# Optimization experiments

Hardware: AMD Instinct MI355X
Metric: run time of the kernel (lower is better)

## Reference

```python
import jax, jax.numpy as jnp
import numpy as np

N, E, CIN, H, HEADS, B = 50000, 800000, 16, 64, 3, 64
D0 = HEADS * H            # conv1 out (heads concatenated) = 192
D1 = D0 + CIN             # x1 dim = 208
D2 = 2 * D1               # x2 dim = 416
MLP_IN = 3 * D2           # 1248
MLP_HID = MLP_IN // 2     # 624
EPS = 1e-5


def setup_inputs() -> dict:
    key = jax.random.key(0)
    ks = jax.random.split(key, 24)
    r = lambda k, s, sc=0.05: (jax.random.normal(k, s, dtype=jnp.float32) * sc)
    inp = {
        'x': jax.random.normal(ks[0], (N, CIN), dtype=jnp.float32),
        'edge_index': jax.random.randint(ks[1], (2, E), 0, N, dtype=jnp.int32),
        'edge_attr': jax.random.normal(ks[2], (E, 4), dtype=jnp.float32),
        'batch': jnp.sort(jax.random.randint(ks[3], (N,), 0, B, dtype=jnp.int32)),
        # conv1 (GeneralConv, heads=3, concat): msg/edge/self linears -> D0
        'W_msg1': r(ks[4], (CIN, D0)), 'b_msg1': jnp.zeros((D0,), jnp.float32),
        'W_edge1': r(ks[5], (4, D0)), 'b_edge1': jnp.zeros((D0,), jnp.float32),
        'W_self1': r(ks[6], (CIN, D0)), 'b_self1': jnp.zeros((D0,), jnp.float32),
        'g1': jnp.ones((D0,), jnp.float32), 'be1': jnp.zeros((D0,), jnp.float32),
        # conv2 (GeneralConv, heads=1, in==out -> identity self)
        'W_msg2': r(ks[7], (D1, D1)), 'b_msg2': jnp.zeros((D1,), jnp.float32),
        'W_edge2': r(ks[8], (4, D1)), 'b_edge2': jnp.zeros((D1,), jnp.float32),
        'g2': jnp.ones((D1,), jnp.float32), 'be2': jnp.zeros((D1,), jnp.float32),
        # MLP head
        'W_l1': r(ks[9], (MLP_IN, MLP_HID)), 'b_l1': jnp.zeros((MLP_HID,), jnp.float32),
        'alpha': jnp.asarray(0.25, jnp.float32),  # PReLU default
        'W_l2': r(ks[10], (MLP_HID, 2)), 'b_l2': jnp.zeros((2,), jnp.float32),
    }
    return inp


def _bn(h, g, b):
    m = h.mean(axis=0)
    v = h.var(axis=0)  # biased, like torch BatchNorm training mode
    return (h - m) * jax.lax.rsqrt(v + EPS) * g + b


def reference(x, edge_index, edge_attr, batch,
              W_msg1, b_msg1, W_edge1, b_edge1, W_self1, b_self1, g1, be1,
              W_msg2, b_msg2, W_edge2, b_edge2, g2, be2,
              W_l1, b_l1, alpha, W_l2, b_l2):
    src, dst = edge_index[0], edge_index[1]
    # conv1: gather -> linear msg + edge feature -> scatter-add -> + self linear
    m1 = x[src] @ W_msg1 + b_msg1 + edge_attr @ W_edge1 + b_edge1   # [E, D0]
    h1 = jax.ops.segment_sum(m1, dst, num_segments=N) + (x @ W_self1 + b_self1)
    h1 = _bn(h1, g1, be1)
    x1 = jnp.concatenate([h1, x], axis=1)                           # [N, D1]
    # conv2 (identity self-connection since in==out)
    m2 = x1[src] @ W_msg2 + b_msg2 + edge_attr @ W_edge2 + b_edge2  # [E, D1]
    h2 = jax.ops.segment_sum(m2, dst, num_segments=N) + x1
    h2 = _bn(h2, g2, be2)
    x2 = jnp.concatenate([h2, x1], axis=1)                          # [N, D2]
    # global add / mean / max pooling by graph id
    s = jax.ops.segment_sum(x2, batch, num_segments=B)
    cnt = jax.ops.segment_sum(jnp.ones((x2.shape[0], 1), x2.dtype), batch, num_segments=B)
    mean = s / jnp.maximum(cnt, 1.0)
    mx = jax.ops.segment_max(x2, batch, num_segments=B)
    pooled = jnp.concatenate([s, mx, mean], axis=1)                 # [B, 3*D2]
    # MLP head: Linear -> Dropout(0) -> PReLU -> Linear -> log_softmax
    h = pooled @ W_l1 + b_l1
    h = jnp.where(h >= 0, h, alpha * h)
    logits = h @ W_l2 + b_l2
    return jax.nn.log_softmax(logits, axis=-1)
```

## Files before the change

### kernel.cpp

```cpp
#include <hip/hip_runtime.h>

typedef __attribute__((ext_vector_type(8))) short short8;
typedef __attribute__((ext_vector_type(4))) float f32x4;
typedef unsigned short u16;
typedef unsigned int u32;

__device__ __forceinline__ u16 f2bf(float f) {
  u32 u = __float_as_uint(f);
  u = (u + 0x7fffu + ((u >> 16) & 1u)) >> 16;
  return (u16)u;
}
__device__ __forceinline__ float bf2f(u16 v) { return __uint_as_float((u32)v << 16); }
__device__ __forceinline__ void atomAddF(float* p, float v) { unsafeAtomicAdd(p, v); }
__device__ __forceinline__ void addp(float* v, u32 p) {
  v[0] += bf2f((u16)p);
  v[1] += bf2f((u16)(p >> 16));
}

__global__ void prep_k(const float* __restrict__ Wm1, const float* __restrict__ We1,
                       const float* __restrict__ Ws1, const float* __restrict__ Wm2,
                       const float* __restrict__ Wl1, const float* __restrict__ x,
                       const int* __restrict__ batch, u16* __restrict__ Wp1,
                       u16* __restrict__ Wp2, u16* __restrict__ Wp3,
                       u16* __restrict__ xbf, int* __restrict__ gstart,
                       int* __restrict__ gend, int* __restrict__ deg,
                       float* __restrict__ bns1p, float* __restrict__ bns2p, int N, int E) {
  int tid = blockIdx.x * 256 + threadIdx.x;
  if (tid < 64 * 192) {
    int k = tid / 192, n = tid % 192;
    float v = 0.f;
    if (k < 16) v = Wm1[k * 192 + n];
    else if (k < 20) v = We1[(k - 16) * 192 + n];
    else if (k < 36) v = Ws1[(k - 20) * 192 + n];
    Wp1[((k >> 3) * 192 + n) * 8 + (k & 7)] = f2bf(v);
  }
  if (tid < 224 * 208) {
    int k = tid / 208, n = tid % 208;
    float v = (k < 208) ? Wm2[k * 208 + n] : 0.f;
    Wp2[((k >> 3) * 208 + n) * 8 + (k & 7)] = f2bf(v);
  }
  if (tid < N * 8) {
    float2 p = *(const float2*)(x + (size_t)tid * 2);
    *(u32*)(xbf + (size_t)tid * 2) = (u32)f2bf(p.x) | ((u32)f2bf(p.y) << 16);
  }
  if (tid < N) {
    int b = batch[tid];
    if (tid == 0 || batch[tid - 1] != b) gstart[b] = tid;
    if (tid == N - 1 || batch[tid + 1] != b) gend[b] = tid;
    deg[tid] = 0;
  }
  if (tid < 64 * 384) bns1p[tid] = 0.f;
  if (tid < 64 * 832) bns2p[tid] = 0.f;
  if (tid < 1248 * 624) {
    int k = tid / 624, n = tid % 624;
    Wp3[((size_t)(k >> 3) * 624 + n) * 8 + (k & 7)] = f2bf(Wl1[(size_t)k * 624 + n]);
  }
}

__global__ void count_k(const int* __restrict__ ei, int* __restrict__ deg,
                        int* __restrict__ ord, int E) {
  int e = blockIdx.x * 256 + threadIdx.x;
  if (e >= E) return;
  ord[e] = atomicAdd(&deg[ei[E + e]], 1);
}

__global__ void scanA_k(const int* __restrict__ deg, int* __restrict__ bsum, int N) {
  __shared__ int sh[256];
  int t = threadIdx.x;
  int i = blockIdx.x * 256 + t;
  sh[t] = (i < N) ? deg[i] : 0;
  __syncthreads();
  for (int off = 128; off > 0; off >>= 1) {
    if (t < off) sh[t] += sh[t + off];
    __syncthreads();
  }
  if (t == 0) bsum[blockIdx.x] = sh[0];
}

__global__ void scanC_k(const int* __restrict__ deg, const int* __restrict__ bsum,
                        int* __restrict__ rowptr, int N, int nb) {
  __shared__ int sb2[256];
  __shared__ int sh[256];
  int t = threadIdx.x;
  int bv = (t < nb) ? bsum[t] : 0;
  sb2[t] = bv;
  __syncthreads();
  for (int off = 1; off < 256; off <<= 1) {
    int u = (t >= off) ? sb2[t - off] : 0;
    __syncthreads();
    sb2[t] += u;
    __syncthreads();
  }
  int bpref = (blockIdx.x == 0) ? 0 : sb2[blockIdx.x - 1];
  int i = blockIdx.x * 256 + t;
  int d = (i < N) ? deg[i] : 0;
  sh[t] = d;
  __syncthreads();
  for (int off = 1; off < 256; off <<= 1) {
    int u = (t >= off) ? sh[t - off] : 0;
    __syncthreads();
    sh[t] += u;
    __syncthreads();
  }
  int excl = sh[t] - d + bpref;
  if (i < N) {
    rowptr[i] = excl;
    if (i == N - 1) rowptr[N] = excl + d;
  }
}

__global__ void scatter_k(const int* __restrict__ ei, const float* __restrict__ ea,
                          const int* __restrict__ ord, const int* __restrict__ rowptr,
                          int4* __restrict__ se16, int E) {
  int e = blockIdx.x * 256 + threadIdx.x;
  if (e >= E) return;
  int s = ei[e], d = ei[E + e];
  float4 w = *(const float4*)(ea + (size_t)e * 4);
  int slot = rowptr[d] + ord[e];
  int4 ent;
  ent.x = s;
  ent.y = (int)((u32)f2bf(w.x) | ((u32)f2bf(w.y) << 16));
  ent.z = (int)((u32)f2bf(w.z) | ((u32)f2bf(w.w) << 16));
  ent.w = 0;
  se16[slot] = ent;
}

__global__ void __launch_bounds__(256) conv1_k(
    const int4* __restrict__ se16, const int* __restrict__ rowptr,
    const u16* __restrict__ xbf, const u16* __restrict__ Bp,
    const float* __restrict__ bm1, const float* __restrict__ be1,
    const float* __restrict__ bs1, u16* __restrict__ acc1c, u16* __restrict__ h1bf,
    float* __restrict__ bns1p, int N) {
  __shared__ __align__(16) u16 Uls[16][72];
  __shared__ float degls[16];
  int tid = threadIdx.x;
  int nl = tid >> 4, q = tid & 15;
  int n = blockIdx.x * 16 + nl;
  bool nval = n < N;
  int j0 = nval ? rowptr[n] : 0;
  int j1 = nval ? rowptr[n + 1] : 0;
  float v[20];
#pragma unroll
  for (int i = 0; i < 20; ++i) v[i] = 0.f;
  {
    int j = j0 + q;
    bool a0 = j < j1, a1 = (j + 16) < j1;
    int jj0 = a0 ? j : 0;
    int jj1 = a1 ? (j + 16) : 0;
    int4 p0 = se16[jj0];
    int4 p1 = se16[jj1];
    const uint4* xs0 = (const uint4*)(xbf + (size_t)(a0 ? p0.x : 0) * 16);
    uint4 x00 = xs0[0], x01 = xs0[1];
    const uint4* xs1 = (const uint4*)(xbf + (size_t)(a1 ? p1.x : 0) * 16);
    uint4 x10 = xs1[0], x11 = xs1[1];
    if (a0) {
      addp(v + 0, x00.x); addp(v + 2, x00.y); addp(v + 4, x00.z); addp(v + 6, x00.w);
      addp(v + 8, x01.x); addp(v + 10, x01.y); addp(v + 12, x01.z); addp(v + 14, x01.w);
      addp(v + 16, (u32)p0.y); addp(v + 18, (u32)p0.z);
    }
    if (a1) {
      addp(v + 0, x10.x); addp(v + 2, x10.y); addp(v + 4, x10.z); addp(v + 6, x10.w);
      addp(v + 8, x11.x); addp(v + 10, x11.y); addp(v + 12, x11.z); addp(v + 14, x11.w);
      addp(v + 16, (u32)p1.y); addp(v + 18, (u32)p1.z);
    }
    for (j += 32; j < j1; j += 16) {
      int4 p = se16[j];
      const uint4* xs = (const uint4*)(xbf + (size_t)p.x * 16);
      uint4 x0 = xs[0], x1 = xs[1];
      addp(v + 0, x0.x); addp(v + 2, x0.y); addp(v + 4, x0.z); addp(v + 6, x0.w);
      addp(v + 8, x1.x); addp(v + 10, x1.y); addp(v + 12, x1.z); addp(v + 14, x1.w);
      addp(v + 16, (u32)p.y); addp(v + 18, (u32)p.z);
    }
  }
#pragma unroll
  for (int i = 0; i < 20; ++i) {
    v[i] += __shfl_xor(v[i], 1);
    v[i] += __shfl_xor(v[i], 2);
    v[i] += __shfl_xor(v[i], 4);
    v[i] += __shfl_xor(v[i], 8);
  }
  float degf = (float)(j1 - j0);
  const u16* xr = xbf + (size_t)n * 16;
  {
    u32 w2[2];
#pragma unroll
    for (int jj = 0; jj < 2; ++jj) {
      int t0 = q * 4 + 2 * jj, t1 = t0 + 1;
      u16 b0 = (t0 < 20) ? f2bf(v[t0]) : ((t0 < 36 && nval) ? xr[t0 - 20] : (u16)0);
      u16 b1 = (t1 < 20) ? f2bf(v[t1]) : ((t1 < 36 && nval) ? xr[t1 - 20] : (u16)0);
      w2[jj] = (u32)b0 | ((u32)b1 << 16);
    }
    *(uint2*)&Uls[nl][q * 4] = make_uint2(w2[0], w2[1]);
  }
  if (nval) {
    int t0 = q * 2, t1 = t0 + 1;
    float f0 = (t0 < 20) ? v[t0] : ((t0 == 20) ? degf : 0.f);
    float f1 = (t1 < 20) ? v[t1] : ((t1 == 20) ? degf : 0.f);
    *(u32*)(acc1c + (size_t)n * 32 + q * 2) = (u32)f2bf(f0) | ((u32)f2bf(f1) << 16);
  }
  if (q == 0) degls[nl] = degf;
  __syncthreads();
  int w = tid >> 6, lane = tid & 63, rc = lane & 15, qd = lane >> 4;
  int slice = (blockIdx.x & 63) * 384;
  for (int nt = w; nt < 12; nt += 4) {
    f32x4 acc = {0.f, 0.f, 0.f, 0.f};
#pragma unroll
    for (int kb = 0; kb < 2; ++kb) {
      short8 av = *(const short8*)&Uls[rc][kb * 32 + qd * 8];
      short8 bv = *(const short8*)(Bp + (size_t)((kb * 4 + qd) * 192 + nt * 16 + rc) * 8);
      acc = __builtin_amdgcn_mfma_f32_16x16x32_bf16(av, bv, acc, 0, 0, 0);
    }
    int col = nt * 16 + rc;
    float bb = bm1[col] + be1[col], bsv = bs1[col];
    float ps = 0.f, pq = 0.f;
#pragma unroll
    for (int r = 0; r < 4; ++r) {
      int ml = qd * 4 + r;
      int m = blockIdx.x * 16 + ml;
      float val = acc[r] + degls[ml] * bb + bsv;
      if (m < N) {
        h1bf[(size_t)m * 192 + col] = f2bf(val);
        ps += val;
        pq += val * val;
      }
    }
    ps += __shfl_xor(ps, 16); ps += __shfl_xor(ps, 32);
    pq += __shfl_xor(pq, 16); pq += __shfl_xor(pq, 32);
    if (qd == 0) {
      atomAddF(&bns1p[slice + col], ps);
      atomAddF(&bns1p[slice + 192 + col], pq);
    }
  }
}

__global__ void bnfin1_k(const float* __restrict__ bns1p, const float* __restrict__ g1,
                         const float* __restrict__ bta1, float Ninv,
                         float* __restrict__ aff1) {
  int c = threadIdx.x;
  if (c >= 192) return;
  float sm = 0.f, sq = 0.f;
  for (int k = 0; k < 64; ++k) {
    sm += bns1p[k * 384 + c];
    sq += bns1p[k * 384 + 192 + c];
  }
  float m1 = sm * Ninv;
  float var = sq * Ninv - m1 * m1;
  float s1 = g1[c] * rsqrtf(var + 1e-5f);
  aff1[c] = s1;
  aff1[192 + c] = bta1[c] - m1 * s1;
}

__global__ void __launch_bounds__(256) conv2_k(
    const int4* __restrict__ se16, const int* __restrict__ rowptr,
    const u16* __restrict__ acc1c, const u16* __restrict__ h1bf,
    const u16* __restrict__ xbf, const u16* __restrict__ Bp1, const u16* __restrict__ Bp2,
    const float* __restrict__ bm1, const float* __restrict__ be1,
    const float* __restrict__ bs1, const float* __restrict__ aff1,
    const float* __restrict__ We2, const float* __restrict__ bm2,
    const float* __restrict__ be2, float* __restrict__ bns2p,
    u16* __restrict__ h2bf, int N) {
  __shared__ __align__(16) u16 Uls[16][72];
  __shared__ __align__(16) u16 Vls[16][232];
  __shared__ __align__(16) u16 X1ls[16][208];
  __shared__ float degls[16], sdegls[16], eals[16][4];
  int tid = threadIdx.x;
  int nl = tid >> 4, q = tid & 15;
  int n = blockIdx.x * 16 + nl;
  bool nval = n < N;
  int j0 = nval ? rowptr[n] : 0;
  int j1 = nval ? rowptr[n + 1] : 0;
  int base = blockIdx.x * 16;

  uint4 sg0, sg1, sgx;
  int r0 = tid / 24, c0 = tid % 24;
  int r1 = (tid + 256) / 24, c1 = (tid + 256) % 24;
  {
    int gr = base + r0;
    sg0 = (gr < N) ? *(const uint4*)(h1bf + (size_t)gr * 192 + c0 * 8)
                   : make_uint4(0, 0, 0, 0);
  }
  if (tid < 128) {
    int gr = base + r1;
    sg1 = (gr < N) ? *(const uint4*)(h1bf + (size_t)gr * 192 + c1 * 8)
                   : make_uint4(0, 0, 0, 0);
  }
  if (tid < 32) {
    int gr = base + (tid >> 1);
    sgx = (gr < N) ? *(const uint4*)(xbf + (size_t)gr * 16 + (tid & 1) * 8)
                   : make_uint4(0, 0, 0, 0);
  }

  float v[21];
#pragma unroll
  for (int i = 0; i < 21; ++i) v[i] = 0.f;
  {
    int j = j0 + q;
    bool a0 = j < j1, a1 = (j + 16) < j1;
    int jj0 = a0 ? j : 0;
    int jj1 = a1 ? (j + 16) : 0;
    int4 p0 = se16[jj0];
    int4 p1 = se16[jj1];
    const uint4* cr0 = (const uint4*)(acc1c + (size_t)(a0 ? p0.x : 0) * 32);
    uint4 c00 = cr0[0], c01 = cr0[1], c02 = cr0[2];
    const uint4* cr1 = (const uint4*)(acc1c + (size_t)(a1 ? p1.x : 0) * 32);
    uint4 c10 = cr1[0], c11 = cr1[1], c12 = cr1[2];
    if (a0) {
      addp(v + 0, c00.x); addp(v + 2, c00.y); addp(v + 4, c00.z); addp(v + 6, c00.w);
      addp(v + 8, c01.x); addp(v + 10, c01.y); addp(v + 12, c01.z); addp(v + 14, c01.w);
      addp(v + 16, c02.x); addp(v + 18, c02.y);
      v[20] += bf2f((u16)c02.z);
    }
    if (a1) {
      addp(v + 0, c10.x); addp(v + 2, c10.y); addp(v + 4, c10.z); addp(v + 6, c10.w);
      addp(v + 8, c11.x); addp(v + 10, c11.y); addp(v + 12, c11.z); addp(v + 14, c11.w);
      addp(v + 16, c12.x); addp(v + 18, c12.y);
      v[20] += bf2f((u16)c12.z);
    }
    for (j += 32; j < j1; j += 16) {
      int s = se16[j].x;
      const uint4* cr = (const uint4*)(acc1c + (size_t)s * 32);
      uint4 c0 = cr[0], c1 = cr[1], c2 = cr[2];
      addp(v + 0, c0.x); addp(v + 2, c0.y); addp(v + 4, c0.z); addp(v + 6, c0.w);
      addp(v + 8, c1.x); addp(v + 10, c1.y); addp(v + 12, c1.z); addp(v + 14, c1.w);
      addp(v + 16, c2.x); addp(v + 18, c2.y);
      v[20] += bf2f((u16)c2.z);
    }
  }

  *(uint4*)&X1ls[r0][c0 * 8] = sg0;
  if (tid < 128) *(uint4*)&X1ls[r1][c1 * 8] = sg1;
  if (tid < 32) *(uint4*)&X1ls[tid >> 1][192 + (tid & 1) * 8] = sgx;

#pragma unroll
  for (int i = 0; i < 21; ++i) {
    v[i] += __shfl_xor(v[i], 1);
    v[i] += __shfl_xor(v[i], 2);
    v[i] += __shfl_xor(v[i], 4);
    v[i] += __shfl_xor(v[i], 8);
  }
  const u16* selfr = acc1c + (size_t)n * 32;
  {
    u32 w2[2];
#pragma unroll
    for (int jj = 0; jj < 2; ++jj) {
      int t0 = q * 4 + 2 * jj, t1 = t0 + 1;
      u16 b0 = (t0 < 20) ? f2bf(v[t0]) : ((t0 < 36 && nval) ? selfr[t0 - 20] : (u16)0);
      u16 b1 = (t1 < 20) ? f2bf(v[t1]) : ((t1 < 36 && nval) ? selfr[t1 - 20] : (u16)0);
      w2[jj] = (u32)b0 | ((u32)b1 << 16);
    }
    *(uint2*)&Uls[nl][q * 4] = make_uint2(w2[0], w2[1]);
  }
  {
    int t0 = q * 2, t1 = t0 + 1;
    u16 b0 = (t0 < 16 && nval) ? selfr[t0] : (u16)0;
    u16 b1 = (t1 < 16 && nval) ? selfr[t1] : (u16)0;
    *(u32*)&Vls[nl][192 + q * 2] = (u32)b0 | ((u32)b1 << 16);
  }
  if (q == 0) sdegls[nl] = v[20];
  if (q == 1) degls[nl] = nval ? bf2f(selfr[20]) : 0.f;
  if (q == 2) {
#pragma unroll
    for (int k = 0; k < 4; ++k) eals[nl][k] = nval ? bf2f(selfr[16 + k]) : 0.f;
  }
  __syncthreads();
  int w = tid >> 6, lane = tid & 63, rc = lane & 15, qd = lane >> 4;
  for (int nt = w; nt < 12; nt += 4) {
    f32x4 acc = {0.f, 0.f, 0.f, 0.f};
#pragma unroll
    for (int kb = 0; kb < 2; ++kb) {
      short8 av = *(const short8*)&Uls[rc][kb * 32 + qd * 8];
      short8 bv = *(const short8*)(Bp1 + (size_t)((kb * 4 + qd) * 192 + nt * 16 + rc) * 8);
      acc = __builtin_amdgcn_mfma_f32_16x16x32_bf16(av, bv, acc, 0, 0, 0);
    }
    int col = nt * 16 + rc;
    float s1 = aff1[col], t1 = aff1[192 + col];
    float bb = bm1[col] + be1[col], bsv = bs1[col];
#pragma unroll
    for (int r = 0; r < 4; ++r) {
      int ml = qd * 4 + r;
      float qv = acc[r] + sdegls[ml] * bb + degls[ml] * bsv;
      Vls[ml][col] = f2bf(qv * s1 + degls[ml] * t1);
    }
  }
  __syncthreads();
  int slice = (blockIdx.x & 63) * 832;
  for (int nt = w; nt < 13; nt += 4) {
    f32x4 acc = {0.f, 0.f, 0.f, 0.f};
#pragma unroll
    for (int kb = 0; kb < 7; ++kb) {
      short8 av = *(const short8*)&Vls[rc][kb * 32 + qd * 8];
      short8 bv = *(const short8*)(Bp2 + (size_t)((kb * 4 + qd) * 208 + nt * 16 + rc) * 8);
      acc = __builtin_amdgcn_mfma_f32_16x16x32_bf16(av, bv, acc, 0, 0, 0);
    }
    int col = nt * 16 + rc;
    float w0 = We2[col], w1 = We2[208 + col], w2 = We2[416 + col], w3 = We2[624 + col];
    float bb2 = bm2[col] + be2[col];
    bool c192 = col < 192;
    float s1 = c192 ? aff1[col] : 0.f;
    float t1 = c192 ? aff1[192 + col] : 0.f;
    float ps = 0.f, pq = 0.f;
#pragma unroll
    for (int r = 0; r < 4; ++r) {
      int ml = qd * 4 + r;
      int m = blockIdx.x * 16 + ml;
      bool mv = m < N;
      float x1 = bf2f(X1ls[ml][col]);
      if (c192) x1 = x1 * s1 + t1;
      float val = acc[r] + eals[ml][0] * w0 + eals[ml][1] * w1 + eals[ml][2] * w2 +
                  eals[ml][3] * w3 + degls[ml] * bb2 + x1;
      if (mv) {
        h2bf[(size_t)m * 208 + col] = f2bf(val);
        ps += val;
        pq += val * val;
      }
    }
    ps += __shfl_xor(ps, 16); ps += __shfl_xor(ps, 32);
    pq += __shfl_xor(pq, 16); pq += __shfl_xor(pq, 32);
    if (qd == 0) {
      atomAddF(&bns2p[slice + col], ps);
      atomAddF(&bns2p[slice + 416 + col], pq);
    }
  }
}

__global__ void bnfin2_k(const float* __restrict__ bns2p, const float* __restrict__ aff1,
                         const float* __restrict__ g2, const float* __restrict__ bta2,
                         float Ninv, float* __restrict__ aff) {
  int f = blockIdx.x * 256 + threadIdx.x;
  if (f >= 416) return;
  float sc, sh;
  if (f < 208) {
    float sm = 0.f, sq = 0.f;
    for (int k = 0; k < 64; ++k) {
      sm += bns2p[k * 832 + f];
      sq += bns2p[k * 832 + 416 + f];
    }
    float m2 = sm * Ninv;
    float var = sq * Ninv - m2 * m2;
    sc = g2[f] * rsqrtf(var + 1e-5f);
    sh = bta2[f] - m2 * sc;
  } else if (f < 400) {
    sc = aff1[f - 208];
    sh = aff1[192 + (f - 208)];
  } else {
    sc = 1.f;
    sh = 0.f;
  }
  aff[f] = sc;
  aff[416 + f] = sh;
}

__global__ void pool_k(const u16* __restrict__ h2bf, const u16* __restrict__ h1bf,
                       const u16* __restrict__ xbf, const float* __restrict__ aff,
                       const int* __restrict__ gstart, const int* __restrict__ gend,
                       float* __restrict__ psp, float* __restrict__ pmp) {
  int b = blockIdx.x, sub = blockIdx.y;
  int t = threadIdx.x;
  if (t >= 208) return;
  int s0 = gstart[b], e0 = gend[b];
  int cnt = (s0 <= e0) ? e0 - s0 + 1 : 0;
  int per = (cnt + 15) >> 4;
  int n0 = s0 + sub * per;
  int n1 = min(n0 + per, s0 + cnt);
  int f = 2 * t;
  const u16* src;
  int stride;
  if (f < 208) { src = h2bf + f; stride = 208; }
  else if (f < 400) { src = h1bf + (f - 208); stride = 192; }
  else { src = xbf + (f - 400); stride = 16; }
  float sc0 = aff[f], sc1 = aff[f + 1];
  float sh0 = aff[416 + f], sh1 = aff[417 + f];
  float s0f = 0.f, s1f = 0.f, m0f = -3.4e38f, m1f = -3.4e38f;
  for (int n = n0; n < n1; ++n) {
    u32 p = *(const u32*)(src + (size_t)n * stride);
    float v0 = bf2f((u16)p) * sc0 + sh0;
    float v1 = bf2f((u16)(p >> 16)) * sc1 + sh1;
    s0f += v0; s1f += v1;
    m0f = fmaxf(m0f, v0); m1f = fmaxf(m1f, v1);
  }
  size_t idx = ((size_t)(b * 16 + sub)) * 416 + f;
  *(float2*)(psp + idx) = make_float2(s0f, s1f);
  *(float2*)(pmp + idx) = make_float2(m0f, m1f);
}

__global__ void pooledprep_k(const float* __restrict__ psp, const float* __restrict__ pmp,
                             const int* __restrict__ gstart, const int* __restrict__ gend,
                             u16* __restrict__ Apool) {
  int b = blockIdx.x, t = threadIdx.x;
  int cnt = gend[b] - gstart[b] + 1;
  float inv = 1.f / (float)max(cnt, 1);
  for (int f = t; f < 416; f += 256) {
    float s = 0.f, m = -3.4e38f;
    for (int k = 0; k < 16; ++k) {
      size_t idx = ((size_t)(b * 16 + k)) * 416 + f;
      s += psp[idx];
      m = fmaxf(m, pmp[idx]);
    }
    u16* row = Apool + (size_t)b * 1248;
    row[f] = f2bf(s);
    row[416 + f] = f2bf((cnt > 0) ? m : 0.f);
    row[832 + f] = f2bf(s * inv);
  }
}

__global__ void mlpgemm_k(const u16* __restrict__ A, const u16* __restrict__ Bp,
                          const float* __restrict__ b1, const float* __restrict__ al,
                          float* __restrict__ hid) {
  int lane = threadIdx.x;
  int mt = blockIdx.x, nt = blockIdx.y;
  int rc = lane & 15, qd = lane >> 4;
  f32x4 acc = {0.f, 0.f, 0.f, 0.f};
  const u16* Ap = A + (size_t)(mt * 16 + rc) * 1248 + qd * 8;
  const u16* Bq = Bp + (size_t)(qd * 624 + nt * 16 + rc) * 8;
  for (int kb = 0; kb < 39; ++kb) {
    short8 av = *(const short8*)(Ap + kb * 32);
    short8 bv = *(const short8*)(Bq + (size_t)kb * 4 * 624 * 8);
    acc = __builtin_amdgcn_mfma_f32_16x16x32_bf16(av, bv, acc, 0, 0, 0);
  }
  int col = nt * 16 + rc;
  float bb = b1[col], alpha = al[0];
  int m0 = mt * 16 + qd * 4;
#pragma unroll
  for (int r = 0; r < 4; ++r) {
    float v = acc[r] + bb;
    hid[(size_t)(m0 + r) * 624 + col] = (v >= 0.f) ? v : alpha * v;
  }
}

__global__ void head_k(const float* __restrict__ hid, const float* __restrict__ W2,
                       const float* __restrict__ b2, float* __restrict__ out) {
  int b = blockIdx.x, t = threadIdx.x;
  float p0 = 0.f, p1 = 0.f;
  for (int k = t; k < 624; k += 64) {
    float h = hid[(size_t)b * 624 + k];
    p0 += h * W2[k * 2];
    p1 += h * W2[k * 2 + 1];
  }
#pragma unroll
  for (int off = 32; off > 0; off >>= 1) {
    p0 += __shfl_down(p0, off);
    p1 += __shfl_down(p1, off);
  }
  if (t == 0) {
    float l0 = p0 + b2[0], l1 = p1 + b2[1];
    float m = fmaxf(l0, l1);
    float lse = m + logf(expf(l0 - m) + expf(l1 - m));
    out[b * 2] = l0 - lse;
    out[b * 2 + 1] = l1 - lse;
  }
}

extern "C" void kernel_launch(void* const* d_in, const int* in_sizes, int n_in,
                              void* d_out, int out_size, void* d_ws, size_t ws_size,
                              hipStream_t stream) {
  const float* x = (const float*)d_in[0];
  const int* ei = (const int*)d_in[1];
  const float* ea = (const float*)d_in[2];
  const int* batch = (const int*)d_in[3];
  const float* Wm1 = (const float*)d_in[4];
  const float* bm1 = (const float*)d_in[5];
  const float* We1 = (const float*)d_in[6];
  const float* be1 = (const float*)d_in[7];
  const float* Ws1 = (const float*)d_in[8];
  const float* bs1 = (const float*)d_in[9];
  const float* g1 = (const float*)d_in[10];
  const float* bta1 = (const float*)d_in[11];
  const float* Wm2 = (const float*)d_in[12];
  const float* bm2 = (const float*)d_in[13];
  const float* We2 = (const float*)d_in[14];
  const float* be2 = (const float*)d_in[15];
  const float* g2 = (const float*)d_in[16];
  const float* bta2 = (const float*)d_in[17];
  const float* Wl1 = (const float*)d_in[18];
  const float* bl1 = (const float*)d_in[19];
  const float* alpha = (const float*)d_in[20];
  const float* Wl2 = (const float*)d_in[21];
  const float* bl2 = (const float*)d_in[22];
  float* out = (float*)d_out;

  const int N = in_sizes[3];
  const int E = in_sizes[2] / 4;
  const int nb = (N + 255) / 256;
  const float Ninv = 1.f / (float)N;

  float* ws = (float*)d_ws;
  size_t o = 0;
  u16* acc1c = (u16*)(ws + o); o += (size_t)N * 16;
  u16* h2bf = (u16*)(ws + o);  o += (size_t)N * 104;
  u16* h1bf = (u16*)(ws + o);  o += (size_t)N * 96;
  u16* xbf = (u16*)(ws + o);   o += (size_t)N * 8;
  u16* Wp1 = (u16*)(ws + o);   o += 6144;
  u16* Wp2 = (u16*)(ws + o);   o += 23296;
  u16* Wp3 = (u16*)(ws + o);   o += 389376;
  u16* Apool = (u16*)(ws + o); o += 39936;
  float* hid = ws + o;    o += 64 * 624;
  float* bns1p = ws + o;  o += 64 * 384;
  float* bns2p = ws + o;  o += 64 * 832;
  float* aff1 = ws + o;   o += 384;
  float* aff = ws + o;    o += 832;
  float* psp = ws + o;    o += (size_t)64 * 16 * 416;
  float* pmp = ws + o;    o += (size_t)64 * 16 * 416;
  int* gstart = (int*)(ws + o); o += 64;
  int* gend = (int*)(ws + o);   o += 64;
  int* deg = (int*)(ws + o);    o += N;
  int* rowptr = (int*)(ws + o); o += N + 1;
  int* ord = (int*)(ws + o);    o += E;
  int* bsum = (int*)(ws + o);   o += 256;
  o = (o + 3) & ~(size_t)3;
  int4* se16 = (int4*)(ws + o); o += (size_t)4 * E;

  const int gconv = (N + 15) / 16;
  prep_k<<<(E + 255) / 256, 256, 0, stream>>>(Wm1, We1, Ws1, Wm2, Wl1, x, batch, Wp1, Wp2,
                                              Wp3, xbf, gstart, gend, deg, bns1p, bns2p,
                                              N, E);
  count_k<<<(E + 255) / 256, 256, 0, stream>>>(ei, deg, ord, E);
  scanA_k<<<nb, 256, 0, stream>>>(deg, bsum, N);
  scanC_k<<<nb, 256, 0, stream>>>(deg, bsum, rowptr, N, nb);
  scatter_k<<<(E + 255) / 256, 256, 0, stream>>>(ei, ea, ord, rowptr, se16, E);
  conv1_k<<<gconv, 256, 0, stream>>>(se16, rowptr, xbf, Wp1, bm1, be1, bs1, acc1c, h1bf,
                                     bns1p, N);
  bnfin1_k<<<1, 256, 0, stream>>>(bns1p, g1, bta1, Ninv, aff1);
  conv2_k<<<gconv, 256, 0, stream>>>(se16, rowptr, acc1c, h1bf, xbf, Wp1, Wp2, bm1, be1,
                                     bs1, aff1, We2, bm2, be2, bns2p, h2bf, N);
  bnfin2_k<<<2, 256, 0, stream>>>(bns2p, aff1, g2, bta2, Ninv, aff);
  pool_k<<<dim3(64, 16), 256, 0, stream>>>(h2bf, h1bf, xbf, aff, gstart, gend, psp, pmp);
  pooledprep_k<<<64, 256, 0, stream>>>(psp, pmp, gstart, gend, Apool);
  mlpgemm_k<<<dim3(4, 39), 64, 0, stream>>>(Apool, Wp3, bl1, alpha, hid);
  head_k<<<64, 64, 0, stream>>>(hid, Wl2, bl2, out);
}
```

Baseline: 292.6 us.

## Double conv node tile to 32 per block and split MLP GEMM K across warps

The conv1 and conv2 kernels now handle 32 nodes per 512-thread block instead of 16 per 256. The MFMA loops are rewritten as jobs over two 16-row tiles, so each fetched weight fragment serves more rows and there are fewer blocks, fewer BN partial-sum atomics per node, and fewer launches. The MLP GEMM now splits its 39-step K loop across four warps and reduces the partial results through shared memory, which shortens the serial MFMA chain per block. In exchange the conv kernels use twice the shared memory and larger blocks, which may reduce occupancy and the scheduler's ability to hide gather latency.

```diff
diff --git a/kernel.cpp b/kernel.cpp
--- a/kernel.cpp
+++ b/kernel.cpp
@@ -125,17 +125,17 @@
   se16[slot] = ent;
 }
 
-__global__ void __launch_bounds__(256) conv1_k(
+__global__ void __launch_bounds__(512) conv1_k(
     const int4* __restrict__ se16, const int* __restrict__ rowptr,
     const u16* __restrict__ xbf, const u16* __restrict__ Bp,
     const float* __restrict__ bm1, const float* __restrict__ be1,
     const float* __restrict__ bs1, u16* __restrict__ acc1c, u16* __restrict__ h1bf,
     float* __restrict__ bns1p, int N) {
-  __shared__ __align__(16) u16 Uls[16][72];
-  __shared__ float degls[16];
+  __shared__ __align__(16) u16 Uls[32][72];
+  __shared__ float degls[32];
   int tid = threadIdx.x;
   int nl = tid >> 4, q = tid & 15;
-  int n = blockIdx.x * 16 + nl;
+  int n = blockIdx.x * 32 + nl;
   bool nval = n < N;
   int j0 = nval ? rowptr[n] : 0;
   int j1 = nval ? rowptr[n + 1] : 0;
@@ -202,11 +202,12 @@
   __syncthreads();
   int w = tid >> 6, lane = tid & 63, rc = lane & 15, qd = lane >> 4;
   int slice = (blockIdx.x & 63) * 384;
-  for (int nt = w; nt < 12; nt += 4) {
+  for (int job = w; job < 24; job += 8) {
+    int mt = job / 12, nt = job % 12;
     f32x4 acc = {0.f, 0.f, 0.f, 0.f};
 #pragma unroll
     for (int kb = 0; kb < 2; ++kb) {
-      short8 av = *(const short8*)&Uls[rc][kb * 32 + qd * 8];
+      short8 av = *(const short8*)&Uls[mt * 16 + rc][kb * 32 + qd * 8];
       short8 bv = *(const short8*)(Bp + (size_t)((kb * 4 + qd) * 192 + nt * 16 + rc) * 8);
       acc = __builtin_amdgcn_mfma_f32_16x16x32_bf16(av, bv, acc, 0, 0, 0);
     }
@@ -215,8 +216,8 @@
     float ps = 0.f, pq = 0.f;
 #pragma unroll
     for (int r = 0; r < 4; ++r) {
-      int ml = qd * 4 + r;
-      int m = blockIdx.x * 16 + ml;
+      int ml = mt * 16 + qd * 4 + r;
+      int m = blockIdx.x * 32 + ml;
       float val = acc[r] + degls[ml] * bb + bsv;
       if (m < N) {
         h1bf[(size_t)m * 192 + col] = f2bf(val);
@@ -250,7 +251,7 @@
   aff1[192 + c] = bta1[c] - m1 * s1;
 }
 
-__global__ void __launch_bounds__(256) conv2_k(
+__global__ void __launch_bounds__(512) conv2_k(
     const int4* __restrict__ se16, const int* __restrict__ rowptr,
     const u16* __restrict__ acc1c, const u16* __restrict__ h1bf,
     const u16* __restrict__ xbf, const u16* __restrict__ Bp1, const u16* __restrict__ Bp2,
@@ -259,32 +260,32 @@
     const float* __restrict__ We2, const float* __restrict__ bm2,
     const float* __restrict__ be2, float* __restrict__ bns2p,
     u16* __restrict__ h2bf, int N) {
-  __shared__ __align__(16) u16 Uls[16][72];
-  __shared__ __align__(16) u16 Vls[16][232];
-  __shared__ __align__(16) u16 X1ls[16][208];
-  __shared__ float degls[16], sdegls[16], eals[16][4];
+  __shared__ __align__(16) u16 Uls[32][72];
+  __shared__ __align__(16) u16 Vls[32][232];
+  __shared__ __align__(16) u16 X1ls[32][208];
+  __shared__ float degls[32], sdegls[32], eals[32][4];
   int tid = threadIdx.x;
   int nl = tid >> 4, q = tid & 15;
-  int n = blockIdx.x * 16 + nl;
+  int n = blockIdx.x * 32 + nl;
   bool nval = n < N;
   int j0 = nval ? rowptr[n] : 0;
   int j1 = nval ? rowptr[n + 1] : 0;
-  int base = blockIdx.x * 16;
+  int base = blockIdx.x * 32;
 
   uint4 sg0, sg1, sgx;
   int r0 = tid / 24, c0 = tid % 24;
-  int r1 = (tid + 256) / 24, c1 = (tid + 256) % 24;
+  int r1 = (tid + 512) / 24, c1 = (tid + 512) % 24;
   {
     int gr = base + r0;
     sg0 = (gr < N) ? *(const uint4*)(h1bf + (size_t)gr * 192 + c0 * 8)
                    : make_uint4(0, 0, 0, 0);
   }
-  if (tid < 128) {
+  if (tid < 256) {
     int gr = base + r1;
     sg1 = (gr < N) ? *(const uint4*)(h1bf + (size_t)gr * 192 + c1 * 8)
                    : make_uint4(0, 0, 0, 0);
   }
-  if (tid < 32) {
+  if (tid < 64) {
     int gr = base + (tid >> 1);
     sgx = (gr < N) ? *(const uint4*)(xbf + (size_t)gr * 16 + (tid & 1) * 8)
                    : make_uint4(0, 0, 0, 0);
@@ -328,8 +329,8 @@
   }
 
   *(uint4*)&X1ls[r0][c0 * 8] = sg0;
-  if (tid < 128) *(uint4*)&X1ls[r1][c1 * 8] = sg1;
-  if (tid < 32) *(uint4*)&X1ls[tid >> 1][192 + (tid & 1) * 8] = sgx;
+  if (tid < 256) *(uint4*)&X1ls[r1][c1 * 8] = sg1;
+  if (tid < 64) *(uint4*)&X1ls[tid >> 1][192 + (tid & 1) * 8] = sgx;
 
 #pragma unroll
   for (int i = 0; i < 21; ++i) {
@@ -364,11 +365,12 @@
   }
   __syncthreads();
   int w = tid >> 6, lane = tid & 63, rc = lane & 15, qd = lane >> 4;
-  for (int nt = w; nt < 12; nt += 4) {
+  for (int job = w; job < 24; job += 8) {
+    int mt = job / 12, nt = job % 12;
     f32x4 acc = {0.f, 0.f, 0.f, 0.f};
 #pragma unroll
     for (int kb = 0; kb < 2; ++kb) {
-      short8 av = *(const short8*)&Uls[rc][kb * 32 + qd * 8];
+      short8 av = *(const short8*)&Uls[mt * 16 + rc][kb * 32 + qd * 8];
       short8 bv = *(const short8*)(Bp1 + (size_t)((kb * 4 + qd) * 192 + nt * 16 + rc) * 8);
       acc = __builtin_amdgcn_mfma_f32_16x16x32_bf16(av, bv, acc, 0, 0, 0);
     }
@@ -377,18 +379,19 @@
     float bb = bm1[col] + be1[col], bsv = bs1[col];
 #pragma unroll
     for (int r = 0; r < 4; ++r) {
-      int ml = qd * 4 + r;
+      int ml = mt * 16 + qd * 4 + r;
       float qv = acc[r] + sdegls[ml] * bb + degls[ml] * bsv;
       Vls[ml][col] = f2bf(qv * s1 + degls[ml] * t1);
     }
   }
   __syncthreads();
   int slice = (blockIdx.x & 63) * 832;
-  for (int nt = w; nt < 13; nt += 4) {
+  for (int job = w; job < 26; job += 8) {
+    int mt = job / 13, nt = job % 13;
     f32x4 acc = {0.f, 0.f, 0.f, 0.f};
 #pragma unroll
     for (int kb = 0; kb < 7; ++kb) {
-      short8 av = *(const short8*)&Vls[rc][kb * 32 + qd * 8];
+      short8 av = *(const short8*)&Vls[mt * 16 + rc][kb * 32 + qd * 8];
       short8 bv = *(const short8*)(Bp2 + (size_t)((kb * 4 + qd) * 208 + nt * 16 + rc) * 8);
       acc = __builtin_amdgcn_mfma_f32_16x16x32_bf16(av, bv, acc, 0, 0, 0);
     }
@@ -401,8 +404,8 @@
     float ps = 0.f, pq = 0.f;
 #pragma unroll
     for (int r = 0; r < 4; ++r) {
-      int ml = qd * 4 + r;
-      int m = blockIdx.x * 16 + ml;
+      int ml = mt * 16 + qd * 4 + r;
+      int m = blockIdx.x * 32 + ml;
       bool mv = m < N;
       float x1 = bf2f(X1ls[ml][col]);
       if (c192) x1 = x1 * s1 + t1;
@@ -503,27 +506,40 @@
   }
 }
 
-__global__ void mlpgemm_k(const u16* __restrict__ A, const u16* __restrict__ Bp,
-                          const float* __restrict__ b1, const float* __restrict__ al,
-                          float* __restrict__ hid) {
-  int lane = threadIdx.x;
+__global__ void __launch_bounds__(256) mlpgemm_k(const u16* __restrict__ A,
+                                                 const u16* __restrict__ Bp,
+                                                 const float* __restrict__ b1,
+                                                 const float* __restrict__ al,
+                                                 float* __restrict__ hid) {
+  __shared__ __align__(16) float part[3][64][4];
+  int tid = threadIdx.x;
+  int w = tid >> 6, lane = tid & 63;
   int mt = blockIdx.x, nt = blockIdx.y;
   int rc = lane & 15, qd = lane >> 4;
   f32x4 acc = {0.f, 0.f, 0.f, 0.f};
   const u16* Ap = A + (size_t)(mt * 16 + rc) * 1248 + qd * 8;
   const u16* Bq = Bp + (size_t)(qd * 624 + nt * 16 + rc) * 8;
-  for (int kb = 0; kb < 39; ++kb) {
+  for (int kb = w; kb < 39; kb += 4) {
     short8 av = *(const short8*)(Ap + kb * 32);
     short8 bv = *(const short8*)(Bq + (size_t)kb * 4 * 624 * 8);
     acc = __builtin_amdgcn_mfma_f32_16x16x32_bf16(av, bv, acc, 0, 0, 0);
   }
-  int col = nt * 16 + rc;
-  float bb = b1[col], alpha = al[0];
-  int m0 = mt * 16 + qd * 4;
-#pragma unroll
-  for (int r = 0; r < 4; ++r) {
-    float v = acc[r] + bb;
-    hid[(size_t)(m0 + r) * 624 + col] = (v >= 0.f) ? v : alpha * v;
+  if (w > 0) *(f32x4*)&part[w - 1][lane][0] = acc;
+  __syncthreads();
+  if (w == 0) {
+#pragma unroll
+    for (int j = 0; j < 3; ++j) {
+      f32x4 p = *(const f32x4*)&part[j][lane][0];
+      acc[0] += p[0]; acc[1] += p[1]; acc[2] += p[2]; acc[3] += p[3];
+    }
+    int col = nt * 16 + rc;
+    float bb = b1[col], alpha = al[0];
+    int m0 = mt * 16 + qd * 4;
+#pragma unroll
+    for (int r = 0; r < 4; ++r) {
+      float v = acc[r] + bb;
+      hid[(size_t)(m0 + r) * 624 + col] = (v >= 0.f) ? v : alpha * v;
+    }
   }
 }
 
@@ -609,7 +625,7 @@
   o = (o + 3) & ~(size_t)3;
   int4* se16 = (int4*)(ws + o); o += (size_t)4 * E;
 
-  const int gconv = (N + 15) / 16;
+  const int gconv = (N + 31) / 32;
   prep_k<<<(E + 255) / 256, 256, 0, stream>>>(Wm1, We1, Ws1, Wm2, Wl1, x, batch, Wp1, Wp2,
                                               Wp3, xbf, gstart, gend, deg, bns1p, bns2p,
                                               N, E);
@@ -617,14 +633,14 @@
   scanA_k<<<nb, 256, 0, stream>>>(deg, bsum, N);
   scanC_k<<<nb, 256, 0, stream>>>(deg, bsum, rowptr, N, nb);
   scatter_k<<<(E + 255) / 256, 256, 0, stream>>>(ei, ea, ord, rowptr, se16, E);
-  conv1_k<<<gconv, 256, 0, stream>>>(se16, rowptr, xbf, Wp1, bm1, be1, bs1, acc1c, h1bf,
+  conv1_k<<<gconv, 512, 0, stream>>>(se16, rowptr, xbf, Wp1, bm1, be1, bs1, acc1c, h1bf,
                                      bns1p, N);
   bnfin1_k<<<1, 256, 0, stream>>>(bns1p, g1, bta1, Ninv, aff1);
-  conv2_k<<<gconv, 256, 0, stream>>>(se16, rowptr, acc1c, h1bf, xbf, Wp1, Wp2, bm1, be1,
+  conv2_k<<<gconv, 512, 0, stream>>>(se16, rowptr, acc1c, h1bf, xbf, Wp1, Wp2, bm1, be1,
                                      bs1, aff1, We2, bm2, be2, bns2p, h2bf, N);
   bnfin2_k<<<2, 256, 0, stream>>>(bns2p, aff1, g2, bta2, Ninv, aff);
   pool_k<<<dim3(64, 16), 256, 0, stream>>>(h2bf, h1bf, xbf, aff, gstart, gend, psp, pmp);
   pooledprep_k<<<64, 256, 0, stream>>>(psp, pmp, gstart, gend, Apool);
-  mlpgemm_k<<<dim3(4, 39), 64, 0, stream>>>(Apool, Wp3, bl1, alpha, hid);
+  mlpgemm_k<<<dim3(4, 39), 256, 0, stream>>>(Apool, Wp3, bl1, alpha, hid);
   head_k<<<64, 64, 0, stream>>>(hid, Wl2, bl2, out);
 }
```

Measured after the change: 289.2 us. Within noise of the previous version (-1.1%).

## Fold BN finalize kernels into conv2 and pooling, split MLP K across waves

Applied to the files above, without the earlier changes.

Removes the two tiny BN-finalize kernels. Every conv2 block now recomputes the BN1 affine into shared memory, and pooledprep computes both BN affines itself. pool_k now pools raw values while also tracking the per-graph min, and the affine is applied afterwards: sum becomes sc*s+cnt*sh, and max uses the min when the scale is negative. mlpgemm is widened to 4 waves that split the K loop and reduce partial sums through LDS. The aim is to cut launch count and serialization, at the cost of each conv2 block redundantly reading the 64x384 partial-stats array and an extra min buffer.

```diff
diff --git a/kernel.cpp b/kernel.cpp
--- a/kernel.cpp
+++ b/kernel.cpp
@@ -233,29 +233,13 @@
   }
 }
 
-__global__ void bnfin1_k(const float* __restrict__ bns1p, const float* __restrict__ g1,
-                         const float* __restrict__ bta1, float Ninv,
-                         float* __restrict__ aff1) {
-  int c = threadIdx.x;
-  if (c >= 192) return;
-  float sm = 0.f, sq = 0.f;
-  for (int k = 0; k < 64; ++k) {
-    sm += bns1p[k * 384 + c];
-    sq += bns1p[k * 384 + 192 + c];
-  }
-  float m1 = sm * Ninv;
-  float var = sq * Ninv - m1 * m1;
-  float s1 = g1[c] * rsqrtf(var + 1e-5f);
-  aff1[c] = s1;
-  aff1[192 + c] = bta1[c] - m1 * s1;
-}
-
 __global__ void __launch_bounds__(256) conv2_k(
     const int4* __restrict__ se16, const int* __restrict__ rowptr,
     const u16* __restrict__ acc1c, const u16* __restrict__ h1bf,
     const u16* __restrict__ xbf, const u16* __restrict__ Bp1, const u16* __restrict__ Bp2,
     const float* __restrict__ bm1, const float* __restrict__ be1,
-    const float* __restrict__ bs1, const float* __restrict__ aff1,
+    const float* __restrict__ bs1, const float* __restrict__ bns1p,
+    const float* __restrict__ g1, const float* __restrict__ bta1, float Ninv,
     const float* __restrict__ We2, const float* __restrict__ bm2,
     const float* __restrict__ be2, float* __restrict__ bns2p,
     u16* __restrict__ h2bf, int N) {
@@ -263,6 +247,7 @@
   __shared__ __align__(16) u16 Vls[16][232];
   __shared__ __align__(16) u16 X1ls[16][208];
   __shared__ float degls[16], sdegls[16], eals[16][4];
+  __shared__ float aff1ls[384];
   int tid = threadIdx.x;
   int nl = tid >> 4, q = tid & 15;
   int n = blockIdx.x * 16 + nl;
@@ -288,6 +273,19 @@
     int gr = base + (tid >> 1);
     sgx = (gr < N) ? *(const uint4*)(xbf + (size_t)gr * 16 + (tid & 1) * 8)
                    : make_uint4(0, 0, 0, 0);
+  }
+
+  if (tid < 192) {
+    float sm = 0.f, sq = 0.f;
+    for (int k = 0; k < 64; ++k) {
+      sm += bns1p[k * 384 + tid];
+      sq += bns1p[k * 384 + 192 + tid];
+    }
+    float m1 = sm * Ninv;
+    float var = sq * Ninv - m1 * m1;
+    float s1 = g1[tid] * rsqrtf(var + 1e-5f);
+    aff1ls[tid] = s1;
+    aff1ls[192 + tid] = bta1[tid] - m1 * s1;
   }
 
   float v[21];
@@ -373,7 +371,7 @@
       acc = __builtin_amdgcn_mfma_f32_16x16x32_bf16(av, bv, acc, 0, 0, 0);
     }
     int col = nt * 16 + rc;
-    float s1 = aff1[col], t1 = aff1[192 + col];
+    float s1 = aff1ls[col], t1 = aff1ls[192 + col];
     float bb = bm1[col] + be1[col], bsv = bs1[col];
 #pragma unroll
     for (int r = 0; r < 4; ++r) {
@@ -396,8 +394,8 @@
     float w0 = We2[col], w1 = We2[208 + col], w2 = We2[416 + col], w3 = We2[624 + col];
     float bb2 = bm2[col] + be2[col];
     bool c192 = col < 192;
-    float s1 = c192 ? aff1[col] : 0.f;
-    float t1 = c192 ? aff1[192 + col] : 0.f;
+    float s1 = c192 ? aff1ls[col] : 0.f;
+    float t1 = c192 ? aff1ls[192 + col] : 0.f;
     float ps = 0.f, pq = 0.f;
 #pragma unroll
     for (int r = 0; r < 4; ++r) {
@@ -423,37 +421,11 @@
   }
 }
 
-__global__ void bnfin2_k(const float* __restrict__ bns2p, const float* __restrict__ aff1,
-                         const float* __restrict__ g2, const float* __restrict__ bta2,
-                         float Ninv, float* __restrict__ aff) {
-  int f = blockIdx.x * 256 + threadIdx.x;
-  if (f >= 416) return;
-  float sc, sh;
-  if (f < 208) {
-    float sm = 0.f, sq = 0.f;
-    for (int k = 0; k < 64; ++k) {
-      sm += bns2p[k * 832 + f];
-      sq += bns2p[k * 832 + 416 + f];
-    }
-    float m2 = sm * Ninv;
-    float var = sq * Ninv - m2 * m2;
-    sc = g2[f] * rsqrtf(var + 1e-5f);
-    sh = bta2[f] - m2 * sc;
-  } else if (f < 400) {
-    sc = aff1[f - 208];
-    sh = aff1[192 + (f - 208)];
-  } else {
-    sc = 1.f;
-    sh = 0.f;
-  }
-  aff[f] = sc;
-  aff[416 + f] = sh;
-}
-
 __global__ void pool_k(const u16* __restrict__ h2bf, const u16* __restrict__ h1bf,
-                       const u16* __restrict__ xbf, const float* __restrict__ aff,
+                       const u16* __restrict__ xbf,
                        const int* __restrict__ gstart, const int* __restrict__ gend,
-                       float* __restrict__ psp, float* __restrict__ pmp) {
+                       float* __restrict__ psp, float* __restrict__ pmp,
+                       float* __restrict__ pnp) {
   int b = blockIdx.x, sub = blockIdx.y;
   int t = threadIdx.x;
   if (t >= 208) return;
@@ -468,62 +440,116 @@
   if (f < 208) { src = h2bf + f; stride = 208; }
   else if (f < 400) { src = h1bf + (f - 208); stride = 192; }
   else { src = xbf + (f - 400); stride = 16; }
-  float sc0 = aff[f], sc1 = aff[f + 1];
-  float sh0 = aff[416 + f], sh1 = aff[417 + f];
-  float s0f = 0.f, s1f = 0.f, m0f = -3.4e38f, m1f = -3.4e38f;
+  float s0f = 0.f, s1f = 0.f;
+  float mx0 = -3.4e38f, mx1 = -3.4e38f, mn0 = 3.4e38f, mn1 = 3.4e38f;
   for (int n = n0; n < n1; ++n) {
     u32 p = *(const u32*)(src + (size_t)n * stride);
-    float v0 = bf2f((u16)p) * sc0 + sh0;
-    float v1 = bf2f((u16)(p >> 16)) * sc1 + sh1;
+    float v0 = bf2f((u16)p);
+    float v1 = bf2f((u16)(p >> 16));
     s0f += v0; s1f += v1;
-    m0f = fmaxf(m0f, v0); m1f = fmaxf(m1f, v1);
+    mx0 = fmaxf(mx0, v0); mx1 = fmaxf(mx1, v1);
+    mn0 = fminf(mn0, v0); mn1 = fminf(mn1, v1);
   }
   size_t idx = ((size_t)(b * 16 + sub)) * 416 + f;
   *(float2*)(psp + idx) = make_float2(s0f, s1f);
-  *(float2*)(pmp + idx) = make_float2(m0f, m1f);
+  *(float2*)(pmp + idx) = make_float2(mx0, mx1);
+  *(float2*)(pnp + idx) = make_float2(mn0, mn1);
 }
 
 __global__ void pooledprep_k(const float* __restrict__ psp, const float* __restrict__ pmp,
+                             const float* __restrict__ pnp,
                              const int* __restrict__ gstart, const int* __restrict__ gend,
-                             u16* __restrict__ Apool) {
+                             const float* __restrict__ bns1p, const float* __restrict__ bns2p,
+                             const float* __restrict__ g1, const float* __restrict__ bta1,
+                             const float* __restrict__ g2, const float* __restrict__ bta2,
+                             float Ninv, u16* __restrict__ Apool) {
+  __shared__ float scs[416], shs[416];
   int b = blockIdx.x, t = threadIdx.x;
+  for (int f = t; f < 416; f += 256) {
+    float sc, sh;
+    if (f < 208) {
+      float sm = 0.f, sq = 0.f;
+      for (int k = 0; k < 64; ++k) {
+        sm += bns2p[k * 832 + f];
+        sq += bns2p[k * 832 + 416 + f];
+      }
+      float m2 = sm * Ninv;
+      float var = sq * Ninv - m2 * m2;
+      sc = g2[f] * rsqrtf(var + 1e-5f);
+      sh = bta2[f] - m2 * sc;
+    } else if (f < 400) {
+      int c = f - 208;
+      float sm = 0.f, sq = 0.f;
+      for (int k = 0; k < 64; ++k) {
+        sm += bns1p[k * 384 + c];
+        sq += bns1p[k * 384 + 192 + c];
+      }
+      float m1 = sm * Ninv;
+      float var = sq * Ninv - m1 * m1;
+      sc = g1[c] * rsqrtf(var + 1e-5f);
+      sh = bta1[c] - m1 * sc;
+    } else {
+      sc = 1.f;
+      sh = 0.f;
+    }
+    scs[f] = sc;
+    shs[f] = sh;
+  }
+  __syncthreads();
   int cnt = gend[b] - gstart[b] + 1;
   float inv = 1.f / (float)max(cnt, 1);
   for (int f = t; f < 416; f += 256) {
-    float s = 0.f, m = -3.4e38f;
+    float s = 0.f, mx = -3.4e38f, mn = 3.4e38f;
     for (int k = 0; k < 16; ++k) {
       size_t idx = ((size_t)(b * 16 + k)) * 416 + f;
       s += psp[idx];
-      m = fmaxf(m, pmp[idx]);
-    }
+      mx = fmaxf(mx, pmp[idx]);
+      mn = fminf(mn, pnp[idx]);
+    }
+    float sc = scs[f], sh = shs[f];
+    float sumf = sc * s + (float)cnt * sh;
+    float mxf = (sc >= 0.f) ? sc * mx + sh : sc * mn + sh;
     u16* row = Apool + (size_t)b * 1248;
-    row[f] = f2bf(s);
-    row[416 + f] = f2bf((cnt > 0) ? m : 0.f);
-    row[832 + f] = f2bf(s * inv);
-  }
-}
-
-__global__ void mlpgemm_k(const u16* __restrict__ A, const u16* __restrict__ Bp,
-                          const float* __restrict__ b1, const float* __restrict__ al,
-                          float* __restrict__ hid) {
-  int lane = threadIdx.x;
+    row[f] = f2bf(sumf);
+    row[416 + f] = f2bf((cnt > 0) ? mxf : 0.f);
+    row[832 + f] = f2bf(sumf * inv);
+  }
+}
+
+__global__ void __launch_bounds__(256) mlpgemm_k(const u16* __restrict__ A,
+                                                 const u16* __restrict__ Bp,
+                                                 const float* __restrict__ b1,
+                                                 const float* __restrict__ al,
+                                                 float* __restrict__ hid) {
+  __shared__ __align__(16) float part[3][64][4];
+  int tid = threadIdx.x;
+  int w = tid >> 6, lane = tid & 63;
   int mt = blockIdx.x, nt = blockIdx.y;
   int rc = lane & 15, qd = lane >> 4;
   f32x4 acc = {0.f, 0.f, 0.f, 0.f};
   const u16* Ap = A + (size_t)(mt * 16 + rc) * 1248 + qd * 8;
   const u16* Bq = Bp + (size_t)(qd * 624 + nt * 16 + rc) * 8;
-  for (int kb = 0; kb < 39; ++kb) {
+  for (int kb = w; kb < 39; kb += 4) {
     short8 av = *(const short8*)(Ap + kb * 32);
     short8 bv = *(const short8*)(Bq + (size_t)kb * 4 * 624 * 8);
     acc = __builtin_amdgcn_mfma_f32_16x16x32_bf16(av, bv, acc, 0, 0, 0);
   }
-  int col = nt * 16 + rc;
-  float bb = b1[col], alpha = al[0];
-  int m0 = mt * 16 + qd * 4;
-#pragma unroll
-  for (int r = 0; r < 4; ++r) {
-    float v = acc[r] + bb;
-    hid[(size_t)(m0 + r) * 624 + col] = (v >= 0.f) ? v : alpha * v;
+  if (w > 0) *(f32x4*)&part[w - 1][lane][0] = acc;
+  __syncthreads();
+  if (w == 0) {
+#pragma unroll
+    for (int j = 0; j < 3; ++j) {
+      f32x4 p = *(const f32x4*)&part[j][lane][0];
+      acc[0] += p[0]; acc[1] += p[1]; acc[2] += p[2]; acc[3] += p[3];
+    }
+    int col = nt * 16 + rc;
+    float bb = b1[col], alpha = al[0];
+    int m0 = mt * 16 + qd * 4;
+#pragma unroll
+    for (int r = 0; r < 4; ++r) {
+      float v = acc[r] + bb;
+      hid[(size_t)(m0 + r) * 624 + col] = (v >= 0.f) ? v : alpha * v;
+    }
   }
 }
 
@@ -596,10 +622,9 @@
   float* hid = ws + o;    o += 64 * 624;
   float* bns1p = ws + o;  o += 64 * 384;
   float* bns2p = ws + o;  o += 64 * 832;
-  float* aff1 = ws + o;   o += 384;
-  float* aff = ws + o;    o += 832;
   float* psp = ws + o;    o += (size_t)64 * 16 * 416;
   float* pmp = ws + o;    o += (size_t)64 * 16 * 416;
+  float* pnp = ws + o;    o += (size_t)64 * 16 * 416;
   int* gstart = (int*)(ws + o); o += 64;
   int* gend = (int*)(ws + o);   o += 64;
   int* deg = (int*)(ws + o);    o += N;
@@ -619,12 +644,12 @@
   scatter_k<<<(E + 255) / 256, 256, 0, stream>>>(ei, ea, ord, rowptr, se16, E);
   conv1_k<<<gconv, 256, 0, stream>>>(se16, rowptr, xbf, Wp1, bm1, be1, bs1, acc1c, h1bf,
                                      bns1p, N);
-  bnfin1_k<<<1, 256, 0, stream>>>(bns1p, g1, bta1, Ninv, aff1);
   conv2_k<<<gconv, 256, 0, stream>>>(se16, rowptr, acc1c, h1bf, xbf, Wp1, Wp2, bm1, be1,
-                                     bs1, aff1, We2, bm2, be2, bns2p, h2bf, N);
-  bnfin2_k<<<2, 256, 0, stream>>>(bns2p, aff1, g2, bta2, Ninv, aff);
-  pool_k<<<dim3(64, 16), 256, 0, stream>>>(h2bf, h1bf, xbf, aff, gstart, gend, psp, pmp);
-  pooledprep_k<<<64, 256, 0, stream>>>(psp, pmp, gstart, gend, Apool);
-  mlpgemm_k<<<dim3(4, 39), 64, 0, stream>>>(Apool, Wp3, bl1, alpha, hid);
+                                     bs1, bns1p, g1, bta1, Ninv, We2, bm2, be2, bns2p,
+                                     h2bf, N);
+  pool_k<<<dim3(64, 16), 256, 0, stream>>>(h2bf, h1bf, xbf, gstart, gend, psp, pmp, pnp);
+  pooledprep_k<<<64, 256, 0, stream>>>(psp, pmp, pnp, gstart, gend, bns1p, bns2p, g1,
+                                       bta1, g2, bta2, Ninv, Apool);
+  mlpgemm_k<<<dim3(4, 39), 256, 0, stream>>>(Apool, Wp3, bl1, alpha, hid);
   head_k<<<64, 64, 0, stream>>>(hid, Wl2, bl2, out);
 }
```

New measurement: 294.5 us. No clear change (+0.7%).
